# Optimization experiments

Measured on AMD Instinct MI355X. Metric: run time of the kernel, lower is better.

Reference implementation:

```python
import jax, jax.numpy as jnp
import numpy as np

N, E, IN_C, HID, OUT_C, L = 50000, 800000, 256, 96, 64, 3
DELTAS = (1.0, 0.5, 0.25)


def setup_inputs() -> dict:
    key = jax.random.key(0)
    ks = jax.random.split(key, 10)
    x = jax.random.normal(ks[0], (N, IN_C), dtype=jnp.float32)
    edge_index = jax.random.randint(ks[1], (2, E), 0, N, dtype=jnp.int64)
    s = 1.0 / np.sqrt(IN_C)
    proj_w = jax.random.uniform(ks[2], (IN_C, HID), jnp.float32, -s, s)
    proj_b = jax.random.uniform(ks[3], (HID,), jnp.float32, -s, s)
    sh = 1.0 / np.sqrt(HID)
    conv_w = jax.random.uniform(ks[4], (L, HID, HID), jnp.float32, -sh, sh)
    conv_b = jnp.zeros((L, HID), dtype=jnp.float32)
    so = 1.0 / np.sqrt(2 * HID)
    out_w = jax.random.uniform(ks[5], (2 * HID, OUT_C), jnp.float32, -so, so)
    out_b = jax.random.uniform(ks[6], (OUT_C,), jnp.float32, -so, so)
    # dithered-quantization uniform noise in (-0.5, 0.5), per layer
    b_noise = jax.random.uniform(ks[7], (L, N, HID), jnp.float32) - 0.5
    # additive gaussian noise, per layer
    eps_noise = jax.random.normal(ks[8], (L, N, HID), dtype=jnp.float32) * 0.01
    return {
        "x": x, "edge_index": edge_index,
        "proj_w": proj_w, "proj_b": proj_b,
        "conv_w": conv_w, "conv_b": conv_b,
        "out_w": out_w, "out_b": out_b,
        "b_noise": b_noise, "eps_noise": eps_noise,
    }


def _gcn_norm(edge_index, n):
    # add self-loops and compute symmetric normalization (PyG gcn_norm)
    loops = jnp.arange(n, dtype=edge_index.dtype)
    src = jnp.concatenate([edge_index[0], loops])
    dst = jnp.concatenate([edge_index[1], loops])
    deg = jax.ops.segment_sum(jnp.ones_like(dst, dtype=jnp.float32), dst, num_segments=n)
    dis = jnp.where(deg > 0, jax.lax.rsqrt(jnp.maximum(deg, 1.0)), 0.0)
    norm = dis[src] * dis[dst]  # [E+N]
    return src, dst, norm


def reference(x, edge_index, proj_w, proj_b, conv_w, conv_b, out_w, out_b, b_noise, eps_noise):
    n = x.shape[0]
    src, dst, norm = _gcn_norm(edge_index, n)
    h0 = x @ proj_w + proj_b  # [N, HID]
    h = h0
    for k in range(L):
        delta = DELTAS[k]
        b = b_noise[k] * delta
        h_q = jnp.floor((h + b) / delta) * delta - b  # dithered quantize
        m = h_q @ conv_w[k]                           # [N, HID]
        agg = jax.ops.segment_sum(m[src] * norm[:, None], dst, num_segments=n)
        h = jax.nn.relu(agg + conv_b[k] + eps_noise[k])
    return jnp.concatenate([h0, h], axis=-1) @ out_w + out_b
```

## Files before the change

### kernel.cpp

```cpp
#include <hip/hip_runtime.h>
#include <math.h>

#define N_NODES 50000
#define N_EDGES 800000
#define IN_C    256
#define HID     96
#define OUT_C   64
#define NLAYER  3
#define KC      96
#define XSP     100


__global__ void k_init(int* cnt, int* cur, int* counter,
                       int* col, float* wgt, int n) {
    int v = blockIdx.x * blockDim.x + threadIdx.x;
    if (v < n) { cnt[v] = 0; cur[v] = 0; }
    if (v == 0) *counter = 0;
    if (v < 8) { col[N_EDGES + v] = 0; wgt[N_EDGES + v] = 0.f; }
}

__global__ void k_count(const int* __restrict__ ei, int* cnt, int e) {
    int i = blockIdx.x * blockDim.x + threadIdx.x;
    if (i < e) atomicAdd(&cnt[ei[e + i]], 1);
}

__global__ void k_node(const int* __restrict__ cnt, float* __restrict__ dis,
                       int* __restrict__ start, int* counter, int n) {
    int v = blockIdx.x * blockDim.x + threadIdx.x;
    if (v < n) {
        int c = cnt[v];
        dis[v] = (float)(1.0 / sqrt((double)(c + 1)));
        start[v] = atomicAdd(counter, c);
    }
}

__global__ void k_fill(const int* __restrict__ ei, const float* __restrict__ dis,
                       const int* __restrict__ start, int* __restrict__ cur,
                       int* __restrict__ col, float* __restrict__ wgt, int e) {
    int i = blockIdx.x * blockDim.x + threadIdx.x;
    if (i < e) {
        int s = ei[i];
        int d = ei[e + i];
        int slot = start[d] + atomicAdd(&cur[d], 1);
        col[slot] = s;
        wgt[slot] = dis[s] * dis[d];
    }
}


template<bool QUANT, bool BIAS>
__global__ __launch_bounds__(384) void k_gemm(
    const float* __restrict__ A, int lda, int K,
    const float* __restrict__ bn, float delta, float inv_delta,
    const float* __restrict__ W, const float* __restrict__ bias,
    float* __restrict__ C)
{
    __shared__ float Ws[KC * HID];
    __shared__ float xs[64 * XSP];
    const int t  = threadIdx.x;
    const int og = t % 24;
    const int rg = t / 24;
    const int nch = (K + KC - 1) / KC;
    const int ngroups = (N_NODES + 63) / 64;

    float4 bv = make_float4(0.f, 0.f, 0.f, 0.f);
    if (BIAS) bv = *(const float4*)&bias[4 * og];

    for (int g = blockIdx.x; g < ngroups; g += gridDim.x) {
        float acc[4][4];
        #pragma unroll
        for (int r = 0; r < 4; r++)
            #pragma unroll
            for (int o = 0; o < 4; o++) acc[r][o] = 0.f;

        for (int ch = 0; ch < nch; ch++) {
            const int kc0 = ch * KC;
            const int kcw = (K - kc0 < KC) ? (K - kc0) : KC;
            __syncthreads();
            for (int i = t; i < 24 * kcw; i += 384) {
                int k = i / 24, oq = i - k * 24;
                *(float4*)&Ws[k * HID + 4 * oq] =
                    *(const float4*)&W[(size_t)(kc0 + k) * HID + 4 * oq];
            }
            const int kq4 = kcw >> 2;
            const int tot = 64 * kq4;
            for (int i = t; i < tot; i += 384) {
                int node, kq;
                if (kq4 == 24) { node = i / 24; kq = i - node * 24; }
                else           { node = i >> 4; kq = i & 15; }
                int gn = g * 64 + node;
                float4 v = make_float4(0.f, 0.f, 0.f, 0.f);
                if (gn < N_NODES) {
                    v = *(const float4*)&A[(size_t)gn * lda + kc0 + 4 * kq];
                    if (QUANT) {
                        float4 b = *(const float4*)&bn[(size_t)gn * HID + kc0 + 4 * kq];
                        float bx = b.x * delta, by = b.y * delta;
                        float bz = b.z * delta, bw = b.w * delta;
                        v.x = floorf((v.x + bx) * inv_delta) * delta - bx;
                        v.y = floorf((v.y + by) * inv_delta) * delta - by;
                        v.z = floorf((v.z + bz) * inv_delta) * delta - bz;
                        v.w = floorf((v.w + bw) * inv_delta) * delta - bw;
                    }
                }
                *(float4*)&xs[node * XSP + 4 * kq] = v;
            }
            __syncthreads();
            for (int k = 0; k < kcw; k += 4) {
                float4 w0 = *(const float4*)&Ws[(k + 0) * HID + 4 * og];
                float4 w1 = *(const float4*)&Ws[(k + 1) * HID + 4 * og];
                float4 w2 = *(const float4*)&Ws[(k + 2) * HID + 4 * og];
                float4 w3 = *(const float4*)&Ws[(k + 3) * HID + 4 * og];
                #pragma unroll
                for (int r = 0; r < 4; r++) {
                    float4 xv = *(const float4*)&xs[(4 * rg + r) * XSP + k];
                    acc[r][0] = fmaf(xv.x, w0.x, acc[r][0]);
                    acc[r][1] = fmaf(xv.x, w0.y, acc[r][1]);
                    acc[r][2] = fmaf(xv.x, w0.z, acc[r][2]);
                    acc[r][3] = fmaf(xv.x, w0.w, acc[r][3]);
                    acc[r][0] = fmaf(xv.y, w1.x, acc[r][0]);
                    acc[r][1] = fmaf(xv.y, w1.y, acc[r][1]);
                    acc[r][2] = fmaf(xv.y, w1.z, acc[r][2]);
                    acc[r][3] = fmaf(xv.y, w1.w, acc[r][3]);
                    acc[r][0] = fmaf(xv.z, w2.x, acc[r][0]);
                    acc[r][1] = fmaf(xv.z, w2.y, acc[r][1]);
                    acc[r][2] = fmaf(xv.z, w2.z, acc[r][2]);
                    acc[r][3] = fmaf(xv.z, w2.w, acc[r][3]);
                    acc[r][0] = fmaf(xv.w, w3.x, acc[r][0]);
                    acc[r][1] = fmaf(xv.w, w3.y, acc[r][1]);
                    acc[r][2] = fmaf(xv.w, w3.z, acc[r][2]);
                    acc[r][3] = fmaf(xv.w, w3.w, acc[r][3]);
                }
            }
        }
        #pragma unroll
        for (int r = 0; r < 4; r++) {
            int gn = g * 64 + 4 * rg + r;
            if (gn < N_NODES) {
                float4 c;
                c.x = acc[r][0] + bv.x;
                c.y = acc[r][1] + bv.y;
                c.z = acc[r][2] + bv.z;
                c.w = acc[r][3] + bv.w;
                *(float4*)&C[(size_t)gn * HID + 4 * og] = c;
            }
        }
    }
}


__global__ __launch_bounds__(384) void k_agg(const float* __restrict__ m,
                                             const int* __restrict__ col,
                                             const float* __restrict__ wgt,
                                             const int* __restrict__ start,
                                             const int* __restrict__ cnt,
                                             const float* __restrict__ dis,
                                             const float* __restrict__ cb,
                                             const float* __restrict__ eps,
                                             float* __restrict__ hout) {
    const int tx = threadIdx.x;
    const int d = blockIdx.x * 4 + threadIdx.y;
    const int s0 = start[d], c = cnt[d];
    const float* mt = m + tx;
    float a0 = 0.f, a1 = 0.f, a2 = 0.f, a3 = 0.f;
    float a4 = 0.f, a5 = 0.f, a6 = 0.f, a7 = 0.f;
    for (int e = 0; e < c; e += 8) {
        int i0 = col[s0 + e + 0]; float w0 = (e + 0 < c) ? wgt[s0 + e + 0] : 0.f;
        int i1 = col[s0 + e + 1]; float w1 = (e + 1 < c) ? wgt[s0 + e + 1] : 0.f;
        int i2 = col[s0 + e + 2]; float w2 = (e + 2 < c) ? wgt[s0 + e + 2] : 0.f;
        int i3 = col[s0 + e + 3]; float w3 = (e + 3 < c) ? wgt[s0 + e + 3] : 0.f;
        int i4 = col[s0 + e + 4]; float w4 = (e + 4 < c) ? wgt[s0 + e + 4] : 0.f;
        int i5 = col[s0 + e + 5]; float w5 = (e + 5 < c) ? wgt[s0 + e + 5] : 0.f;
        int i6 = col[s0 + e + 6]; float w6 = (e + 6 < c) ? wgt[s0 + e + 6] : 0.f;
        int i7 = col[s0 + e + 7]; float w7 = (e + 7 < c) ? wgt[s0 + e + 7] : 0.f;
        a0 = fmaf(mt[i0 * HID], w0, a0);
        a1 = fmaf(mt[i1 * HID], w1, a1);
        a2 = fmaf(mt[i2 * HID], w2, a2);
        a3 = fmaf(mt[i3 * HID], w3, a3);
        a4 = fmaf(mt[i4 * HID], w4, a4);
        a5 = fmaf(mt[i5 * HID], w5, a5);
        a6 = fmaf(mt[i6 * HID], w6, a6);
        a7 = fmaf(mt[i7 * HID], w7, a7);
    }
    float dv = dis[d];
    float a = ((a0 + a1) + (a2 + a3)) + ((a4 + a5) + (a6 + a7));
    a = fmaf(mt[d * HID], dv * dv, a);
    a += cb[tx] + eps[(size_t)d * HID + tx];
    hout[(size_t)d * HID + tx] = fmaxf(a, 0.f);
}


__global__ __launch_bounds__(256) void k_out(const float* __restrict__ h0,
                                             const float* __restrict__ h,
                                             const float* __restrict__ W,
                                             const float* __restrict__ bias,
                                             float* __restrict__ out) {
    __shared__ float Ws[2 * HID * OUT_C];
    __shared__ float cs[4][2 * HID];
    int tx = threadIdx.x, ty = threadIdx.y;
    int t = ty * OUT_C + tx;
    for (int i = t; i < 2 * HID * OUT_C; i += 256) Ws[i] = W[i];
    __syncthreads();
    const int ng = N_NODES / 4;
    for (int g = blockIdx.x; g < ng; g += gridDim.x) {
        int r = g * 4 + ty;
        for (int i = tx; i < HID; i += OUT_C) {
            cs[ty][i] = h0[r * HID + i];
            cs[ty][HID + i] = h[r * HID + i];
        }
        __syncthreads();
        float a = 0.f;
        #pragma unroll 16
        for (int i = 0; i < 2 * HID; i++) a = fmaf(cs[ty][i], Ws[i * OUT_C + tx], a);
        out[r * OUT_C + tx] = a + bias[tx];
        __syncthreads();
    }
}


extern "C" void kernel_launch(void* const* d_in, const int* in_sizes, int n_in,
                              void* d_out, int out_size, void* d_ws, size_t ws_size,
                              hipStream_t stream) {
    (void)in_sizes; (void)n_in; (void)out_size; (void)ws_size;
    const float* x       = (const float*)d_in[0];
    const int*   ei      = (const int*)d_in[1];
    const float* proj_w  = (const float*)d_in[2];
    const float* proj_b  = (const float*)d_in[3];
    const float* conv_w  = (const float*)d_in[4];
    const float* conv_b  = (const float*)d_in[5];
    const float* out_w   = (const float*)d_in[6];
    const float* out_b   = (const float*)d_in[7];
    const float* b_noise = (const float*)d_in[8];
    const float* eps_n   = (const float*)d_in[9];
    float*       out     = (float*)d_out;

    char* w = (char*)d_ws;
    size_t off = 0;
    auto alloc = [&](size_t bytes) -> char* {
        char* p = w + off;
        off = (off + bytes + 255) & ~(size_t)255;
        return p;
    };
    float* h0b   = (float*)alloc((size_t)N_NODES * HID * 4);
    float* hA    = (float*)alloc((size_t)N_NODES * HID * 4);
    float* mb    = (float*)alloc((size_t)N_NODES * HID * 4);
    float* dis   = (float*)alloc((size_t)N_NODES * 4);
    float* wgt   = (float*)alloc((size_t)(N_EDGES + 8) * 4);
    int*   col   = (int*)  alloc((size_t)(N_EDGES + 8) * 4);
    int*   cnt   = (int*)  alloc((size_t)N_NODES * 4);
    int*   cur   = (int*)  alloc((size_t)N_NODES * 4);
    int*   start = (int*)  alloc((size_t)N_NODES * 4);
    int*   ctr   = (int*)  alloc(256);

    k_init <<<(N_NODES + 255) / 256, 256, 0, stream>>>(cnt, cur, ctr, col, wgt, N_NODES);
    k_count<<<(N_EDGES + 255) / 256, 256, 0, stream>>>(ei, cnt, N_EDGES);
    k_node <<<(N_NODES + 255) / 256, 256, 0, stream>>>(cnt, dis, start, ctr, N_NODES);
    k_fill <<<(N_EDGES + 255) / 256, 256, 0, stream>>>(ei, dis, start, cur, col, wgt, N_EDGES);

    const int ngroups = (N_NODES + 63) / 64;

    k_gemm<false, true><<<ngroups, 384, 0, stream>>>(
        x, IN_C, IN_C, nullptr, 1.f, 1.f, proj_w, proj_b, h0b);

    const float deltas[NLAYER] = {1.0f, 0.5f, 0.25f};
    const float* hprev = h0b;
    for (int k = 0; k < NLAYER; k++) {
        float dlt = deltas[k];
        k_gemm<true, false><<<ngroups, 384, 0, stream>>>(
            hprev, HID, HID,
            b_noise + (size_t)k * N_NODES * HID, dlt, 1.0f / dlt,
            conv_w + (size_t)k * HID * HID, nullptr, mb);
        k_agg<<<N_NODES / 4, dim3(96, 4), 0, stream>>>(
            mb, col, wgt, start, cnt, dis,
            conv_b + (size_t)k * HID,
            eps_n + (size_t)k * N_NODES * HID, hA);
        hprev = hA;
    }

    k_out<<<1024, dim3(64, 4), 0, stream>>>(h0b, hprev, out_w, out_b, out);
}
```

Before: 715.0 us.

## Fuse dithered quantization into producer epilogues and reuse GEMM for output layer

Dithered quantization moves out of the GEMM's A-tile loading and into the epilogue of the previous producer. The projection GEMM now writes both h0 and the quantized layer-0 input, and each aggregation kernel writes the quantized input for the next layer. The aggregation kernel now processes float2 per thread with 8 nodes per block, and the custom output kernel is replaced by the templated tiled GEMM that reads h0 and h as two K-segments. The GEMMs are also compile-time specialized with fully unrolled K chunks. This removes redundant quantization work and per-element loop overhead, but it adds an extra write of the quantized buffer in the projection step.

```diff
diff --git a/kernel.cpp b/kernel.cpp
--- a/kernel.cpp
+++ b/kernel.cpp
@@ -7,8 +7,6 @@
 #define HID     96
 #define OUT_C   64
 #define NLAYER  3
-#define KC      96
-#define XSP     100
 
 
 __global__ void k_init(int* cnt, int* cur, int* counter,
@@ -48,121 +46,123 @@
 }
 
 
-template<bool QUANT, bool BIAS>
-__global__ __launch_bounds__(384) void k_gemm(
-    const float* __restrict__ A, int lda, int K,
+template<int KTOT, int KC, int NOUT, bool BIAS, bool WRITEQ>
+__global__ __launch_bounds__((NOUT / 4) * 16) void k_gemm(
+    const float* __restrict__ A1, int lda, int K1,
+    const float* __restrict__ A2,
+    const float* __restrict__ W, const float* __restrict__ bias,
     const float* __restrict__ bn, float delta, float inv_delta,
-    const float* __restrict__ W, const float* __restrict__ bias,
-    float* __restrict__ C)
+    float* __restrict__ C, float* __restrict__ Cq)
 {
-    __shared__ float Ws[KC * HID];
-    __shared__ float xs[64 * XSP];
-    const int t  = threadIdx.x;
-    const int og = t % 24;
-    const int rg = t / 24;
-    const int nch = (K + KC - 1) / KC;
-    const int ngroups = (N_NODES + 63) / 64;
-
+    constexpr int OG    = NOUT / 4;
+    constexpr int BLOCK = OG * 16;
+    constexpr int XSTR  = KC + 4;
+    __shared__ float Ws[KC * NOUT];
+    __shared__ float xs[64 * XSTR];
+
+    const int t    = threadIdx.x;
+    const int og   = t % OG;
+    const int rg   = t / OG;
+    const int base = blockIdx.x * 64;
+
+    float acc[4][4];
+    #pragma unroll
+    for (int r = 0; r < 4; r++)
+        #pragma unroll
+        for (int o = 0; o < 4; o++) acc[r][o] = 0.f;
+
+    #pragma unroll
+    for (int ch = 0; ch < KTOT / KC; ch++) {
+        const int kc0 = ch * KC;
+        const float* Asrc = A1;
+        int acol = kc0, alda = lda;
+        if (kc0 >= K1) { Asrc = A2; acol = kc0 - K1; alda = HID; }
+        __syncthreads();
+        for (int i = t; i < KC * OG; i += BLOCK) {
+            int k = i / OG, oq = i % OG;
+            *(float4*)&Ws[k * NOUT + 4 * oq] =
+                *(const float4*)&W[(size_t)(kc0 + k) * NOUT + 4 * oq];
+        }
+        for (int i = t; i < 64 * (KC / 4); i += BLOCK) {
+            int node = i / (KC / 4), kq = i % (KC / 4);
+            int gn = base + node;
+            float4 v = make_float4(0.f, 0.f, 0.f, 0.f);
+            if (gn < N_NODES)
+                v = *(const float4*)&Asrc[(size_t)gn * alda + acol + 4 * kq];
+            *(float4*)&xs[node * XSTR + 4 * kq] = v;
+        }
+        __syncthreads();
+        #pragma unroll
+        for (int k = 0; k < KC; k += 4) {
+            float4 w0 = *(const float4*)&Ws[(k + 0) * NOUT + 4 * og];
+            float4 w1 = *(const float4*)&Ws[(k + 1) * NOUT + 4 * og];
+            float4 w2 = *(const float4*)&Ws[(k + 2) * NOUT + 4 * og];
+            float4 w3 = *(const float4*)&Ws[(k + 3) * NOUT + 4 * og];
+            #pragma unroll
+            for (int r = 0; r < 4; r++) {
+                float4 xv = *(const float4*)&xs[(4 * rg + r) * XSTR + k];
+                acc[r][0] = fmaf(xv.x, w0.x, acc[r][0]);
+                acc[r][1] = fmaf(xv.x, w0.y, acc[r][1]);
+                acc[r][2] = fmaf(xv.x, w0.z, acc[r][2]);
+                acc[r][3] = fmaf(xv.x, w0.w, acc[r][3]);
+                acc[r][0] = fmaf(xv.y, w1.x, acc[r][0]);
+                acc[r][1] = fmaf(xv.y, w1.y, acc[r][1]);
+                acc[r][2] = fmaf(xv.y, w1.z, acc[r][2]);
+                acc[r][3] = fmaf(xv.y, w1.w, acc[r][3]);
+                acc[r][0] = fmaf(xv.z, w2.x, acc[r][0]);
+                acc[r][1] = fmaf(xv.z, w2.y, acc[r][1]);
+                acc[r][2] = fmaf(xv.z, w2.z, acc[r][2]);
+                acc[r][3] = fmaf(xv.z, w2.w, acc[r][3]);
+                acc[r][0] = fmaf(xv.w, w3.x, acc[r][0]);
+                acc[r][1] = fmaf(xv.w, w3.y, acc[r][1]);
+                acc[r][2] = fmaf(xv.w, w3.z, acc[r][2]);
+                acc[r][3] = fmaf(xv.w, w3.w, acc[r][3]);
+            }
+        }
+    }
     float4 bv = make_float4(0.f, 0.f, 0.f, 0.f);
     if (BIAS) bv = *(const float4*)&bias[4 * og];
-
-    for (int g = blockIdx.x; g < ngroups; g += gridDim.x) {
-        float acc[4][4];
-        #pragma unroll
-        for (int r = 0; r < 4; r++)
-            #pragma unroll
-            for (int o = 0; o < 4; o++) acc[r][o] = 0.f;
-
-        for (int ch = 0; ch < nch; ch++) {
-            const int kc0 = ch * KC;
-            const int kcw = (K - kc0 < KC) ? (K - kc0) : KC;
-            __syncthreads();
-            for (int i = t; i < 24 * kcw; i += 384) {
-                int k = i / 24, oq = i - k * 24;
-                *(float4*)&Ws[k * HID + 4 * oq] =
-                    *(const float4*)&W[(size_t)(kc0 + k) * HID + 4 * oq];
+    #pragma unroll
+    for (int r = 0; r < 4; r++) {
+        int gn = base + 4 * rg + r;
+        if (gn < N_NODES) {
+            float4 c;
+            c.x = acc[r][0] + bv.x;
+            c.y = acc[r][1] + bv.y;
+            c.z = acc[r][2] + bv.z;
+            c.w = acc[r][3] + bv.w;
+            *(float4*)&C[(size_t)gn * NOUT + 4 * og] = c;
+            if (WRITEQ) {
+                float4 b = *(const float4*)&bn[(size_t)gn * NOUT + 4 * og];
+                float bx = b.x * delta, by = b.y * delta;
+                float bz = b.z * delta, bw = b.w * delta;
+                float4 q;
+                q.x = floorf((c.x + bx) * inv_delta) * delta - bx;
+                q.y = floorf((c.y + by) * inv_delta) * delta - by;
+                q.z = floorf((c.z + bz) * inv_delta) * delta - bz;
+                q.w = floorf((c.w + bw) * inv_delta) * delta - bw;
+                *(float4*)&Cq[(size_t)gn * NOUT + 4 * og] = q;
             }
-            const int kq4 = kcw >> 2;
-            const int tot = 64 * kq4;
-            for (int i = t; i < tot; i += 384) {
-                int node, kq;
-                if (kq4 == 24) { node = i / 24; kq = i - node * 24; }
-                else           { node = i >> 4; kq = i & 15; }
-                int gn = g * 64 + node;
-                float4 v = make_float4(0.f, 0.f, 0.f, 0.f);
-                if (gn < N_NODES) {
-                    v = *(const float4*)&A[(size_t)gn * lda + kc0 + 4 * kq];
-                    if (QUANT) {
-                        float4 b = *(const float4*)&bn[(size_t)gn * HID + kc0 + 4 * kq];
-                        float bx = b.x * delta, by = b.y * delta;
-                        float bz = b.z * delta, bw = b.w * delta;
-                        v.x = floorf((v.x + bx) * inv_delta) * delta - bx;
-                        v.y = floorf((v.y + by) * inv_delta) * delta - by;
-                        v.z = floorf((v.z + bz) * inv_delta) * delta - bz;
-                        v.w = floorf((v.w + bw) * inv_delta) * delta - bw;
-                    }
-                }
-                *(float4*)&xs[node * XSP + 4 * kq] = v;
-            }
-            __syncthreads();
-            for (int k = 0; k < kcw; k += 4) {
-                float4 w0 = *(const float4*)&Ws[(k + 0) * HID + 4 * og];
-                float4 w1 = *(const float4*)&Ws[(k + 1) * HID + 4 * og];
-                float4 w2 = *(const float4*)&Ws[(k + 2) * HID + 4 * og];
-                float4 w3 = *(const float4*)&Ws[(k + 3) * HID + 4 * og];
-                #pragma unroll
-                for (int r = 0; r < 4; r++) {
-                    float4 xv = *(const float4*)&xs[(4 * rg + r) * XSP + k];
-                    acc[r][0] = fmaf(xv.x, w0.x, acc[r][0]);
-                    acc[r][1] = fmaf(xv.x, w0.y, acc[r][1]);
-                    acc[r][2] = fmaf(xv.x, w0.z, acc[r][2]);
-                    acc[r][3] = fmaf(xv.x, w0.w, acc[r][3]);
-                    acc[r][0] = fmaf(xv.y, w1.x, acc[r][0]);
-                    acc[r][1] = fmaf(xv.y, w1.y, acc[r][1]);
-                    acc[r][2] = fmaf(xv.y, w1.z, acc[r][2]);
-                    acc[r][3] = fmaf(xv.y, w1.w, acc[r][3]);
-                    acc[r][0] = fmaf(xv.z, w2.x, acc[r][0]);
-                    acc[r][1] = fmaf(xv.z, w2.y, acc[r][1]);
-                    acc[r][2] = fmaf(xv.z, w2.z, acc[r][2]);
-                    acc[r][3] = fmaf(xv.z, w2.w, acc[r][3]);
-                    acc[r][0] = fmaf(xv.w, w3.x, acc[r][0]);
-                    acc[r][1] = fmaf(xv.w, w3.y, acc[r][1]);
-                    acc[r][2] = fmaf(xv.w, w3.z, acc[r][2]);
-                    acc[r][3] = fmaf(xv.w, w3.w, acc[r][3]);
-                }
-            }
-        }
-        #pragma unroll
-        for (int r = 0; r < 4; r++) {
-            int gn = g * 64 + 4 * rg + r;
-            if (gn < N_NODES) {
-                float4 c;
-                c.x = acc[r][0] + bv.x;
-                c.y = acc[r][1] + bv.y;
-                c.z = acc[r][2] + bv.z;
-                c.w = acc[r][3] + bv.w;
-                *(float4*)&C[(size_t)gn * HID + 4 * og] = c;
-            }
-        }
-    }
-}
-
-
-__global__ __launch_bounds__(384) void k_agg(const float* __restrict__ m,
-                                             const int* __restrict__ col,
-                                             const float* __restrict__ wgt,
-                                             const int* __restrict__ start,
-                                             const int* __restrict__ cnt,
-                                             const float* __restrict__ dis,
-                                             const float* __restrict__ cb,
-                                             const float* __restrict__ eps,
-                                             float* __restrict__ hout) {
+        }
+    }
+}
+
+
+template<bool QUANT>
+__global__ __launch_bounds__(384) void k_agg(
+    const float* __restrict__ m, const int* __restrict__ col,
+    const float* __restrict__ wgt, const int* __restrict__ start,
+    const int* __restrict__ cnt, const float* __restrict__ dis,
+    const float* __restrict__ cb, const float* __restrict__ eps,
+    const float* __restrict__ bn, float delta, float inv_delta,
+    float* __restrict__ hout)
+{
     const int tx = threadIdx.x;
-    const int d = blockIdx.x * 4 + threadIdx.y;
+    const int d  = blockIdx.x * 8 + threadIdx.y;
     const int s0 = start[d], c = cnt[d];
-    const float* mt = m + tx;
-    float a0 = 0.f, a1 = 0.f, a2 = 0.f, a3 = 0.f;
-    float a4 = 0.f, a5 = 0.f, a6 = 0.f, a7 = 0.f;
+    const float2* mt = (const float2*)m + tx;
+    float2 a0 = {0.f, 0.f}, a1 = {0.f, 0.f}, a2 = {0.f, 0.f}, a3 = {0.f, 0.f};
+    float2 a4 = {0.f, 0.f}, a5 = {0.f, 0.f}, a6 = {0.f, 0.f}, a7 = {0.f, 0.f};
     for (int e = 0; e < c; e += 8) {
         int i0 = col[s0 + e + 0]; float w0 = (e + 0 < c) ? wgt[s0 + e + 0] : 0.f;
         int i1 = col[s0 + e + 1]; float w1 = (e + 1 < c) ? wgt[s0 + e + 1] : 0.f;
@@ -172,48 +172,40 @@
         int i5 = col[s0 + e + 5]; float w5 = (e + 5 < c) ? wgt[s0 + e + 5] : 0.f;
         int i6 = col[s0 + e + 6]; float w6 = (e + 6 < c) ? wgt[s0 + e + 6] : 0.f;
         int i7 = col[s0 + e + 7]; float w7 = (e + 7 < c) ? wgt[s0 + e + 7] : 0.f;
-        a0 = fmaf(mt[i0 * HID], w0, a0);
-        a1 = fmaf(mt[i1 * HID], w1, a1);
-        a2 = fmaf(mt[i2 * HID], w2, a2);
-        a3 = fmaf(mt[i3 * HID], w3, a3);
-        a4 = fmaf(mt[i4 * HID], w4, a4);
-        a5 = fmaf(mt[i5 * HID], w5, a5);
-        a6 = fmaf(mt[i6 * HID], w6, a6);
-        a7 = fmaf(mt[i7 * HID], w7, a7);
+        float2 v0 = mt[(size_t)i0 * 48], v1 = mt[(size_t)i1 * 48];
+        float2 v2 = mt[(size_t)i2 * 48], v3 = mt[(size_t)i3 * 48];
+        float2 v4 = mt[(size_t)i4 * 48], v5 = mt[(size_t)i5 * 48];
+        float2 v6 = mt[(size_t)i6 * 48], v7 = mt[(size_t)i7 * 48];
+        a0.x = fmaf(v0.x, w0, a0.x); a0.y = fmaf(v0.y, w0, a0.y);
+        a1.x = fmaf(v1.x, w1, a1.x); a1.y = fmaf(v1.y, w1, a1.y);
+        a2.x = fmaf(v2.x, w2, a2.x); a2.y = fmaf(v2.y, w2, a2.y);
+        a3.x = fmaf(v3.x, w3, a3.x); a3.y = fmaf(v3.y, w3, a3.y);
+        a4.x = fmaf(v4.x, w4, a4.x); a4.y = fmaf(v4.y, w4, a4.y);
+        a5.x = fmaf(v5.x, w5, a5.x); a5.y = fmaf(v5.y, w5, a5.y);
+        a6.x = fmaf(v6.x, w6, a6.x); a6.y = fmaf(v6.y, w6, a6.y);
+        a7.x = fmaf(v7.x, w7, a7.x); a7.y = fmaf(v7.y, w7, a7.y);
     }
     float dv = dis[d];
-    float a = ((a0 + a1) + (a2 + a3)) + ((a4 + a5) + (a6 + a7));
-    a = fmaf(mt[d * HID], dv * dv, a);
-    a += cb[tx] + eps[(size_t)d * HID + tx];
-    hout[(size_t)d * HID + tx] = fmaxf(a, 0.f);
-}
-
-
-__global__ __launch_bounds__(256) void k_out(const float* __restrict__ h0,
-                                             const float* __restrict__ h,
-                                             const float* __restrict__ W,
-                                             const float* __restrict__ bias,
-                                             float* __restrict__ out) {
-    __shared__ float Ws[2 * HID * OUT_C];
-    __shared__ float cs[4][2 * HID];
-    int tx = threadIdx.x, ty = threadIdx.y;
-    int t = ty * OUT_C + tx;
-    for (int i = t; i < 2 * HID * OUT_C; i += 256) Ws[i] = W[i];
-    __syncthreads();
-    const int ng = N_NODES / 4;
-    for (int g = blockIdx.x; g < ng; g += gridDim.x) {
-        int r = g * 4 + ty;
-        for (int i = tx; i < HID; i += OUT_C) {
-            cs[ty][i] = h0[r * HID + i];
-            cs[ty][HID + i] = h[r * HID + i];
-        }
-        __syncthreads();
-        float a = 0.f;
-        #pragma unroll 16
-        for (int i = 0; i < 2 * HID; i++) a = fmaf(cs[ty][i], Ws[i * OUT_C + tx], a);
-        out[r * OUT_C + tx] = a + bias[tx];
-        __syncthreads();
-    }
+    float sw = dv * dv;
+    float2 sv = mt[(size_t)d * 48];
+    float ax = ((a0.x + a1.x) + (a2.x + a3.x)) + ((a4.x + a5.x) + (a6.x + a7.x));
+    float ay = ((a0.y + a1.y) + (a2.y + a3.y)) + ((a4.y + a5.y) + (a6.y + a7.y));
+    ax = fmaf(sv.x, sw, ax);
+    ay = fmaf(sv.y, sw, ay);
+    float2 cbv = ((const float2*)cb)[tx];
+    float2 ev  = ((const float2*)eps)[(size_t)d * 48 + tx];
+    float hx = fmaxf(ax + cbv.x + ev.x, 0.f);
+    float hy = fmaxf(ay + cbv.y + ev.y, 0.f);
+    float2 o;
+    if (QUANT) {
+        float2 b = ((const float2*)bn)[(size_t)d * 48 + tx];
+        float bx = b.x * delta, by = b.y * delta;
+        o.x = floorf((hx + bx) * inv_delta) * delta - bx;
+        o.y = floorf((hy + by) * inv_delta) * delta - by;
+    } else {
+        o.x = hx; o.y = hy;
+    }
+    ((float2*)hout)[(size_t)d * 48 + tx] = o;
 }
 
 
@@ -241,7 +233,7 @@
         return p;
     };
     float* h0b   = (float*)alloc((size_t)N_NODES * HID * 4);
-    float* hA    = (float*)alloc((size_t)N_NODES * HID * 4);
+    float* hq    = (float*)alloc((size_t)N_NODES * HID * 4);
     float* mb    = (float*)alloc((size_t)N_NODES * HID * 4);
     float* dis   = (float*)alloc((size_t)N_NODES * 4);
     float* wgt   = (float*)alloc((size_t)(N_EDGES + 8) * 4);
@@ -257,24 +249,31 @@
     k_fill <<<(N_EDGES + 255) / 256, 256, 0, stream>>>(ei, dis, start, cur, col, wgt, N_EDGES);
 
     const int ngroups = (N_NODES + 63) / 64;
-
-    k_gemm<false, true><<<ngroups, 384, 0, stream>>>(
-        x, IN_C, IN_C, nullptr, 1.f, 1.f, proj_w, proj_b, h0b);
-
     const float deltas[NLAYER] = {1.0f, 0.5f, 0.25f};
-    const float* hprev = h0b;
+
+    k_gemm<256, 32, HID, true, true><<<ngroups, 384, 0, stream>>>(
+        x, IN_C, 256, nullptr, proj_w, proj_b,
+        b_noise, deltas[0], 1.0f / deltas[0], h0b, hq);
+
     for (int k = 0; k < NLAYER; k++) {
-        float dlt = deltas[k];
-        k_gemm<true, false><<<ngroups, 384, 0, stream>>>(
-            hprev, HID, HID,
-            b_noise + (size_t)k * N_NODES * HID, dlt, 1.0f / dlt,
-            conv_w + (size_t)k * HID * HID, nullptr, mb);
-        k_agg<<<N_NODES / 4, dim3(96, 4), 0, stream>>>(
-            mb, col, wgt, start, cnt, dis,
-            conv_b + (size_t)k * HID,
-            eps_n + (size_t)k * N_NODES * HID, hA);
-        hprev = hA;
-    }
-
-    k_out<<<1024, dim3(64, 4), 0, stream>>>(h0b, hprev, out_w, out_b, out);
-}
+        k_gemm<96, 48, HID, false, false><<<ngroups, 384, 0, stream>>>(
+            hq, HID, 96, nullptr, conv_w + (size_t)k * HID * HID, nullptr,
+            nullptr, 0.f, 0.f, mb, nullptr);
+        if (k < NLAYER - 1) {
+            k_agg<true><<<N_NODES / 8, dim3(48, 8), 0, stream>>>(
+                mb, col, wgt, start, cnt, dis,
+                conv_b + (size_t)k * HID, eps_n + (size_t)k * N_NODES * HID,
+                b_noise + (size_t)(k + 1) * N_NODES * HID,
+                deltas[k + 1], 1.0f / deltas[k + 1], hq);
+        } else {
+            k_agg<false><<<N_NODES / 8, dim3(48, 8), 0, stream>>>(
+                mb, col, wgt, start, cnt, dis,
+                conv_b + (size_t)k * HID, eps_n + (size_t)k * N_NODES * HID,
+                nullptr, 0.f, 0.f, hq);
+        }
+    }
+
+    k_gemm<192, 48, OUT_C, true, false><<<ngroups, 256, 0, stream>>>(
+        h0b, HID, 96, hq, out_w, out_b,
+        nullptr, 0.f, 0.f, out, nullptr);
+}
```

Measured after the change: 1.030 ms. 1.44x slower.
